# Kernel optimization log

Measured on AMD Instinct MI355X. Metric: run time of the kernel, lower is better.

## Reference

```python
import jax, jax.numpy as jnp
import numpy as np

SEGMENT_LENGTHS = (768, 1536, 3072, 6144, 12288)
DILATED_RATIOS = (1, 2, 4, 8, 16)
NUM_HEADS = 12
NEG_INF = -1e9


def _layer_norm(x, g, b, eps=1e-5):
    mu = jnp.mean(x, axis=-1, keepdims=True)
    var = jnp.mean((x - mu) ** 2, axis=-1, keepdims=True)
    return (x - mu) * jax.lax.rsqrt(var + eps) * g + b


def _dilated_branch(q, k, v, w, r):
    # q,k,v: (B, L, H, Dh); segment length w, dilation ratio r (w % r == 0)
    B, L, H, Dh = q.shape
    Lp = -(-L // w) * w
    n, m = Lp // w, w // r
    gsz = -(-H // r)  # head-group size (heads padded up to a multiple of r in LongNet)
    offs = jnp.arange(H) // gsz  # per-head token offset within each r-block
    oh = jax.nn.one_hot(offs, r, dtype=q.dtype)  # (H, r)

    def gather(t):
        t = jnp.pad(t, ((0, 0), (0, Lp - L), (0, 0), (0, 0)))
        t = t.reshape(B, n, m, r, H, Dh)  # segments of w = m blocks of r
        return jnp.einsum('bnmrhd,hr->bnmhd', t, oh)  # each head picks its offset

    qi, ki, vi = gather(q), gather(k), gather(v)
    s = jnp.einsum('bnihd,bnjhd->bnhij', qi * (Dh ** -0.5), ki)  # (B,n,H,m,m)
    lse = jax.scipy.special.logsumexp(s, axis=-1)  # (B,n,H,m)
    o = jnp.einsum('bnhij,bnjhd->bnihd', jax.nn.softmax(s, axis=-1), vi)
    # scatter back to dense token positions; uncovered slots get 0 / -inf lse
    o_full = jnp.einsum('bnmhd,hr->bnmrhd', o, oh).reshape(B, Lp, H, Dh)
    lse = jnp.transpose(lse, (0, 1, 3, 2))  # (B,n,m,H)
    lse_full = jnp.where(oh.T[None, None, None] > 0, lse[:, :, :, None, :], NEG_INF)
    lse_full = lse_full.reshape(B, Lp, H)
    return o_full[:, :L], lse_full[:, :L]


def _dilated_attention(q, k, v):
    outs, lses = [], []
    for w, r in zip(SEGMENT_LENGTHS, DILATED_RATIOS):
        o, l = _dilated_branch(q, k, v, w, r)
        outs.append(o)
        lses.append(l)
    lse = jnp.stack(lses)  # (n_branch, B, L, H)
    wts = jnp.exp(lse - lse.max(0))
    wts = wts / wts.sum(0)  # softmax-combine branches by their lse (LongNet recombination)
    return (jnp.stack(outs) * wts[..., None]).sum(0)  # (B, L, H, Dh)


def _forward(x, patch_w, patch_b, cls_token, pos_embed,
             ln1_g, ln1_b, wq, bq, wk, bk, wv, bv, wo, bo,
             ln2_g, ln2_b, w1, b1, w2, b2, normf_g, normf_b, head_w, head_b):
    B, Cin, D, Hs, Ws = x.shape
    E = patch_w.shape[0]
    pd, ph, pw = patch_w.shape[2], patch_w.shape[3], patch_w.shape[4]
    # non-overlapping 3D patch embed (Conv3d with stride == kernel)
    xp = x.reshape(B, Cin, D // pd, pd, Hs // ph, ph, Ws // pw, pw)
    tok = jnp.einsum('bcxpyqzr,ecpqr->bxyze', xp, patch_w).reshape(B, -1, E) + patch_b
    tok = tok + pos_embed[:, 1:]
    cls = cls_token + pos_embed[:, :1]
    h = jnp.concatenate([jnp.broadcast_to(cls, (B, 1, E)), tok], axis=1)
    L = h.shape[1]
    Dh = E // NUM_HEADS
    depth = wq.shape[0]
    for i in range(depth):  # pre-LN transformer layers with LongNet dilated attention
        hn = _layer_norm(h, ln1_g[i], ln1_b[i])
        q = (hn @ wq[i] + bq[i]).reshape(B, L, NUM_HEADS, Dh)
        k = (hn @ wk[i] + bk[i]).reshape(B, L, NUM_HEADS, Dh)
        v = (hn @ wv[i] + bv[i]).reshape(B, L, NUM_HEADS, Dh)
        a = _dilated_attention(q, k, v).reshape(B, L, E)
        h = h + a @ wo[i] + bo[i]
        hn = _layer_norm(h, ln2_g[i], ln2_b[i])
        h = h + jax.nn.gelu(hn @ w1[i] + b1[i], approximate=False) @ w2[i] + b2[i]
    h = _layer_norm(h, normf_g, normf_b)
    return h[:, 0] @ head_w + head_b  # (B, num_classes)


def setup_inputs() -> dict:
    key = jax.random.key(0)
    ks = jax.random.split(key, 12)
    B, E, depth, ncls = 2, 768, 2, 1000
    D, Hs, Ws = 48, 256, 256
    N = (D // 4) * (Hs // 16) * (Ws // 16)  # 3072 patches
    f32 = jnp.float32
    s = 0.02
    return {
        'x': jax.random.normal(ks[0], (B, 1, D, Hs, Ws), f32),
        'patch_w': jax.random.normal(ks[1], (E, 1, 4, 16, 16), f32) * s,
        'patch_b': jnp.zeros((E,), f32),
        'cls_token': jax.random.normal(ks[2], (1, 1, E), f32) * s,
        'pos_embed': jax.random.normal(ks[3], (1, N + 1, E), f32) * s,
        'ln1_g': jnp.ones((depth, E), f32),
        'ln1_b': jnp.zeros((depth, E), f32),
        'wq': jax.random.normal(ks[4], (depth, E, E), f32) * s,
        'bq': jnp.zeros((depth, E), f32),
        'wk': jax.random.normal(ks[5], (depth, E, E), f32) * s,
        'bk': jnp.zeros((depth, E), f32),
        'wv': jax.random.normal(ks[6], (depth, E, E), f32) * s,
        'bv': jnp.zeros((depth, E), f32),
        'wo': jax.random.normal(ks[7], (depth, E, E), f32) * s,
        'bo': jnp.zeros((depth, E), f32),
        'ln2_g': jnp.ones((depth, E), f32),
        'ln2_b': jnp.zeros((depth, E), f32),
        'w1': jax.random.normal(ks[8], (depth, E, 4 * E), f32) * s,
        'b1': jnp.zeros((depth, 4 * E), f32),
        'w2': jax.random.normal(ks[9], (depth, 4 * E, E), f32) * s,
        'b2': jnp.zeros((depth, E), f32),
        'normf_g': jnp.ones((E,), f32),
        'normf_b': jnp.zeros((E,), f32),
        'head_w': jax.random.normal(ks[10], (E, ncls), f32) * s,
        'head_b': jnp.zeros((ncls,), f32),
    }


def reference(x, patch_w, patch_b, cls_token, pos_embed,
              ln1_g, ln1_b, wq, bq, wk, bk, wv, bv, wo, bo,
              ln2_g, ln2_b, w1, b1, w2, b2, normf_g, normf_b, head_w, head_b):
    return _forward(x, patch_w, patch_b, cls_token, pos_embed,
                    ln1_g, ln1_b, wq, bq, wk, bk, wv, bv, wo, bo,
                    ln2_g, ln2_b, w1, b1, w2, b2, normf_g, normf_b, head_w, head_b)
```

## Files before the change

kernel.cpp:

```cpp
#include <hip/hip_runtime.h>
#include <math.h>

#define TOK_L 3073
#define EMB 768
#define NH 12
#define DH 64
#define BATCH 2
#define QKVS 2304
#define HSZ ((size_t)BATCH * TOK_L * EMB)
#define MHC ((size_t)BATCH * TOK_L * NH)

typedef __bf16 bf16;
typedef __bf16 v8bf __attribute__((ext_vector_type(8)));
typedef __bf16 v4bf __attribute__((ext_vector_type(4)));
typedef float  v4f  __attribute__((ext_vector_type(4)));

__device__ __forceinline__ v8bf zero8() {
    v8bf v;
    #pragma unroll
    for (int i = 0; i < 8; i++) v[i] = (bf16)0.f;
    return v;
}
__device__ __forceinline__ v4f zero4() {
    v4f v; v[0] = 0.f; v[1] = 0.f; v[2] = 0.f; v[3] = 0.f; return v;
}
__device__ __forceinline__ float gelu_f(float x) {
    return 0.5f * x * (1.0f + erff(x * 0.70710678118654752f));
}
__device__ __forceinline__ void gload16(const bf16* g, bf16* l) {
    __builtin_amdgcn_global_load_lds(
        (const __attribute__((address_space(1))) void*)g,
        (__attribute__((address_space(3))) void*)l, 16, 0, 0);
}

__device__ __forceinline__ void convT_tile(const float* __restrict__ src,
                                           bf16* __restrict__ dst,
                                           int K, int N, int tx, int ty)
{
    __shared__ float t[32][33];
    int n0 = tx * 32, k0 = ty * 32;
    int r = threadIdx.x >> 3, c4 = (threadIdx.x & 7) * 4;
    float4 v = *(const float4*)(src + (size_t)(k0 + r) * N + n0 + c4);
    t[r][c4 + 0] = v.x; t[r][c4 + 1] = v.y; t[r][c4 + 2] = v.z; t[r][c4 + 3] = v.w;
    __syncthreads();
    v4bf o;
    o[0] = (bf16)t[c4 + 0][r]; o[1] = (bf16)t[c4 + 1][r];
    o[2] = (bf16)t[c4 + 2][r]; o[3] = (bf16)t[c4 + 3][r];
    *(v4bf*)(dst + (size_t)(n0 + r) * K + k0 + c4) = o;
}

__global__ __launch_bounds__(256) void prep_weights(
    const float* __restrict__ wq, const float* __restrict__ wk,
    const float* __restrict__ wv, const float* __restrict__ wo,
    const float* __restrict__ w1, const float* __restrict__ w2,
    const float* __restrict__ patch_w,
    bf16* __restrict__ qkv_t0, bf16* __restrict__ wo_t0,
    bf16* __restrict__ w1_t, bf16* __restrict__ w2_t, bf16* __restrict__ pw_b)
{
    int bid = blockIdx.x;
    if (bid >= 13824) {
        int i = ((bid - 13824) * 256 + threadIdx.x) * 4;
        float4 v = *(const float4*)(patch_w + i);
        v4bf o; o[0] = (bf16)v.x; o[1] = (bf16)v.y; o[2] = (bf16)v.z; o[3] = (bf16)v.w;
        *(v4bf*)(pw_b + i) = o;
        return;
    }
    int layer = bid / 6912, t = bid % 6912;
    if (t < 1728) {
        int m = t / 576, tt = t % 576;
        const float* src = (m == 0 ? wq : m == 1 ? wk : wv) + (size_t)layer * 589824;
        bf16* dst = qkv_t0 + (size_t)layer * QKVS * 768 + (size_t)m * 589824;
        convT_tile(src, dst, 768, 768, tt % 24, tt / 24);
    } else if (t < 2304) {
        int tt = t - 1728;
        convT_tile(wo + (size_t)layer * 589824, wo_t0 + (size_t)layer * 589824,
                   768, 768, tt % 24, tt / 24);
    } else if (t < 4608) {
        int tt = t - 2304;
        convT_tile(w1 + (size_t)layer * 2359296, w1_t + (size_t)layer * 2359296,
                   768, 3072, tt % 96, tt / 96);
    } else {
        int tt = t - 4608;
        convT_tile(w2 + (size_t)layer * 2359296, w2_t + (size_t)layer * 2359296,
                   3072, 768, tt % 24, tt / 24);
    }
}

__global__ __launch_bounds__(256) void prep_small(const float* __restrict__ bq,
    const float* __restrict__ bk, const float* __restrict__ bv, float* __restrict__ d,
    const float* __restrict__ cls, const float* __restrict__ pos, float* __restrict__ h)
{
    int i = blockIdx.x * 256 + threadIdx.x;
    if (i < 2 * QKVS) {
        int layer = i / QKVS, j = i % QKVS;
        const float* s = (j < 768) ? bq : (j < 1536) ? bk : bv;
        d[i] = s[(size_t)layer * 768 + (j & 767)];
    }
    if (i < 2 * 768) {
        int b = i / 768, e = i % 768;
        h[(size_t)b * TOK_L * EMB + e] = cls[e] + pos[e];
    }
}

__global__ __launch_bounds__(256) void gather_patches(const float* __restrict__ x,
                                                      bf16* __restrict__ Xp) {
    int p = blockIdx.x;
    int b = p / 3072, pp = p % 3072;
    int px = pp >> 8, py = (pp >> 4) & 15, pz = pp & 15;
    for (int k = threadIdx.x; k < 1024; k += 256) {
        int pd = k >> 8, ph = (k >> 4) & 15, pw = k & 15;
        size_t src = ((size_t)(b * 48 + px * 4 + pd)) * 65536
                   + (size_t)(py * 16 + ph) * 256 + (size_t)(pz * 16 + pw);
        Xp[(size_t)p * 1024 + k] = (bf16)x[src];
    }
}

template<int BN>
__global__ __launch_bounds__(256) void gemm_bf16(
    const bf16* __restrict__ A, const bf16* __restrict__ Bt,
    const float* __restrict__ bias, float* __restrict__ Cf,
    bf16* __restrict__ Cb, int M, int N, int K, int flags,
    const float* __restrict__ pos)
{
    __shared__ bf16 As[128 * 32];
    __shared__ bf16 Bs[BN * 32];
    const int tid = threadIdx.x;
    const int lane = tid & 63, wid = tid >> 6;
    const int ln15 = lane & 15, q4 = lane >> 4;
    const int m0 = blockIdx.y * 128, n0 = blockIdx.x * BN;
    const int wm = (wid & 1) * 64, wn = (wid >> 1) * (BN / 2);
    const int srow = lane >> 2;
    const int schunk = (lane & 3) * 8;
    const int NF = BN / 32;

    v4f acc[4][NF];
    #pragma unroll
    for (int i = 0; i < 4; i++)
        #pragma unroll
        for (int j = 0; j < NF; j++) acc[i][j] = zero4();

    for (int k0 = 0; k0 < K; k0 += 32) {
        #pragma unroll
        for (int i = 0; i < 2; i++) {
            int rg = wid * 32 + i * 16;
            int gm = m0 + rg + srow; if (gm >= M) gm = M - 1;
            gload16(A + (size_t)gm * K + k0 + schunk, As + rg * 32);
        }
        if (BN == 128) {
            #pragma unroll
            for (int i = 0; i < 2; i++) {
                int rg = wid * 32 + i * 16;
                gload16(Bt + (size_t)(n0 + rg + srow) * K + k0 + schunk, Bs + rg * 32);
            }
        } else {
            int rg = wid * 16;
            gload16(Bt + (size_t)(n0 + rg + srow) * K + k0 + schunk, Bs + rg * 32);
        }
        __syncthreads();
        v8bf af[4], bfr[NF];
        #pragma unroll
        for (int mt = 0; mt < 4; mt++)
            af[mt] = *(const v8bf*)(As + (wm + mt * 16 + ln15) * 32 + q4 * 8);
        #pragma unroll
        for (int nt = 0; nt < NF; nt++)
            bfr[nt] = *(const v8bf*)(Bs + (wn + nt * 16 + ln15) * 32 + q4 * 8);
        #pragma unroll
        for (int mt = 0; mt < 4; mt++)
            #pragma unroll
            for (int nt = 0; nt < NF; nt++)
                acc[mt][nt] = __builtin_amdgcn_mfma_f32_16x16x32_bf16(af[mt], bfr[nt], acc[mt][nt], 0, 0, 0);
        __syncthreads();
    }
    #pragma unroll
    for (int mt = 0; mt < 4; mt++) {
        #pragma unroll
        for (int nt = 0; nt < NF; nt++) {
            #pragma unroll
            for (int g = 0; g < 4; g++) {
                int row = m0 + wm + mt * 16 + q4 * 4 + g;
                if (row >= M) continue;
                int col = n0 + wn + nt * 16 + ln15;
                float v = acc[mt][nt][g] + bias[col];
                if (flags & 2) v = gelu_f(v);
                size_t crow;
                if (flags & 4) {
                    int rowp = row % 3072;
                    crow = (size_t)(row + row / 3072 + 1);
                    v += pos[(size_t)(rowp + 1) * EMB + col];
                } else crow = (size_t)row;
                size_t ci = crow * (size_t)N + col;
                if (flags & 8) Cb[ci] = (bf16)v;
                else { if (flags & 1) v += Cf[ci]; Cf[ci] = v; }
            }
        }
    }
}

__global__ __launch_bounds__(256) void layernorm_kernel(
    const float* __restrict__ x, const float* __restrict__ g,
    const float* __restrict__ bb, bf16* __restrict__ y, int nrows)
{
    int row = blockIdx.x;
    if (row >= nrows) return;
    int tid = threadIdx.x;
    const float* xr = x + (size_t)row * EMB;
    float v0 = xr[tid], v1 = xr[tid + 256], v2 = xr[tid + 512];
    __shared__ float red[256];
    red[tid] = v0 + v1 + v2;
    __syncthreads();
    for (int o = 128; o > 0; o >>= 1) { if (tid < o) red[tid] += red[tid + o]; __syncthreads(); }
    float mu = red[0] * (1.f / 768.f);
    __syncthreads();
    float d0 = v0 - mu, d1 = v1 - mu, d2 = v2 - mu;
    red[tid] = d0 * d0 + d1 * d1 + d2 * d2;
    __syncthreads();
    for (int o = 128; o > 0; o >>= 1) { if (tid < o) red[tid] += red[tid + o]; __syncthreads(); }
    float rs = rsqrtf(red[0] * (1.f / 768.f) + 1e-5f);
    bf16* yr = y + (size_t)row * EMB;
    yr[tid]       = (bf16)(d0 * rs * g[tid]       + bb[tid]);
    yr[tid + 256] = (bf16)(d1 * rs * g[tid + 256] + bb[tid + 256]);
    yr[tid + 512] = (bf16)(d2 * rs * g[tid + 512] + bb[tid + 512]);
}

__global__ __launch_bounds__(256) void pack_vt(const bf16* __restrict__ qkv,
                                               bf16* __restrict__ Vt)
{
    __shared__ bf16 t[64 * 65];
    int yy = blockIdx.y;
    int br, seg;
    if (yy < 5)       { br = 0; seg = yy; }
    else if (yy < 8)  { br = 1; seg = yy - 5; }
    else if (yy < 10) { br = 2; seg = yy - 8; }
    else if (yy == 10){ br = 3; seg = 0; }
    else              { br = 4; seg = 0; }
    const int r = 1 << br, w = 768 << br;
    const int gsz = (NH + r - 1) / r;
    const int bh = blockIdx.z;
    const int b = bh / NH, hd = bh % NH;
    const int off = hd / gsz;
    const int kbase = seg * w + off;
    const int kt = blockIdx.x;
    const int tid = threadIdx.x;
    const int dq = (tid & 7) * 8;
    #pragma unroll
    for (int p = 0; p < 2; p++) {
        int jl = (tid >> 3) + p * 32;
        int pk = kbase + (kt * 64 + jl) * r;
        v8bf val = (pk < TOK_L)
            ? *(const v8bf*)(qkv + (size_t)(b * TOK_L + pk) * QKVS + 1536 + hd * DH + dq)
            : zero8();
        #pragma unroll
        for (int i = 0; i < 8; i++) t[jl * 65 + dq + i] = val[i];
    }
    __syncthreads();
    #pragma unroll
    for (int p = 0; p < 2; p++) {
        int d = (tid >> 3) + p * 32;
        int kk = (tid & 7) * 8;
        v8bf o;
        #pragma unroll
        for (int i = 0; i < 8; i++) o[i] = t[(kk + i) * 65 + d];
        *(v8bf*)(Vt + ((size_t)(yy * 24 + bh) * 64 + d) * 768 + kt * 64 + kk) = o;
    }
}

__global__ __launch_bounds__(256) void attn_mfma(
    const bf16* __restrict__ qkv, const bf16* __restrict__ Vt,
    bf16* __restrict__ oac, bf16* __restrict__ obr, float* __restrict__ lse5)
{
    __shared__ bf16 kl[2 * 4096];
    __shared__ bf16 pl[4][32 * 72];
    const int tid = threadIdx.x;
    const int lane = tid & 63, wid = tid >> 6;
    const int ln15 = lane & 15, q4 = lane >> 4;
    const int bid = blockIdx.x;
    const int xcd = bid & 7, rest = bid >> 3;
    const int slot = rest / 6, t = rest - slot * 6;
    const int g = (slot << 3) | xcd;
    const int yy = g / 24, bh = g - yy * 24;
    int br, seg;
    if (yy < 5)       { br = 0; seg = yy; }
    else if (yy < 8)  { br = 1; seg = yy - 5; }
    else if (yy < 10) { br = 2; seg = yy - 8; }
    else if (yy == 10){ br = 3; seg = 0; }
    else              { br = 4; seg = 0; }
    const int r = 1 << br, w = 768 << br;
    const int gsz = (NH + r - 1) / r;
    const int b = bh / NH, hd = bh % NH;
    const int off = hd / gsz;
    const int sbase = seg * w + off;
    if (sbase + (t * 128) * r >= TOK_L) return;

    int n_valid = (TOK_L - sbase + r - 1) / r;
    if (n_valid > 768) n_valid = 768;
    const int kt_lim = (n_valid + 63) >> 6;
    const float pad_add = (float)(768 - n_valid);
    const int qoff = t * 128 + wid * 32;
    const bool wactive = (sbase + qoff * r) < TOK_L;

    const bf16* qb_ = qkv + hd * DH;
    const bf16* kb_ = qkv + 768 + hd * DH;

    auto stageK = [&](int ktv, int bufi) {
        #pragma unroll
        for (int p = 0; p < 2; p++) {
            int row = (tid >> 3) + p * 32;
            int pk = sbase + (ktv * 64 + row) * r;
            if (pk >= TOK_L) pk = 0;
            gload16(kb_ + (size_t)(b * TOK_L + pk) * QKVS + (tid & 7) * 8,
                    kl + bufi * 4096 + wid * 512 + p * 2048);
        }
    };

    v8bf qf[2][2];
    #pragma unroll
    for (int mt = 0; mt < 2; mt++) {
        int pq = sbase + (qoff + mt * 16 + ln15) * r;
        #pragma unroll
        for (int ks = 0; ks < 2; ks++) {
            v8bf qv = (pq < TOK_L)
                ? *(const v8bf*)(qb_ + (size_t)(b * TOK_L + pq) * QKVS + ks * 32 + q4 * 8)
                : zero8();
            #pragma unroll
            for (int i = 0; i < 8; i++) qv[i] = (bf16)((float)qv[i] * 0.125f);
            qf[mt][ks] = qv;
        }
    }
    v4f o[2][4];
    float lsum[2][4];
    #pragma unroll
    for (int mt = 0; mt < 2; mt++)
        #pragma unroll
        for (int g2 = 0; g2 < 4; g2++) { lsum[mt][g2] = 0.f; o[mt][g2] = zero4(); }
    #pragma unroll
    for (int mt = 0; mt < 2; mt++)
        #pragma unroll
        for (int dt = 0; dt < 4; dt++) o[mt][dt] = zero4();

    const bf16* vtb = Vt + (size_t)(yy * 24 + bh) * 64 * 768;
    bf16* plw = &pl[wid][0];

    stageK(0, 0);
    __syncthreads();

    for (int kt = 0; kt < kt_lim; kt++) {
        const int cur = kt & 1;
        if (kt + 1 < kt_lim) stageK(kt + 1, cur ^ 1);
        if (wactive) {
            const bf16* klc = kl + cur * 4096;
            v8bf kf[4][2];
            #pragma unroll
            for (int nt = 0; nt < 4; nt++)
                #pragma unroll
                for (int ks = 0; ks < 2; ks++)
                    kf[nt][ks] = *(const v8bf*)(klc + (nt * 16 + ln15) * 64 + ks * 32 + q4 * 8);
            v4f s[2][4];
            #pragma unroll
            for (int mt = 0; mt < 2; mt++)
                #pragma unroll
                for (int nt = 0; nt < 4; nt++) {
                    s[mt][nt] = __builtin_amdgcn_mfma_f32_16x16x32_bf16(qf[mt][0], kf[nt][0], zero4(), 0, 0, 0);
                    s[mt][nt] = __builtin_amdgcn_mfma_f32_16x16x32_bf16(qf[mt][1], kf[nt][1], s[mt][nt], 0, 0, 0);
                }
            bool vm[4];
            #pragma unroll
            for (int nt = 0; nt < 4; nt++)
                vm[nt] = (kt * 64 + nt * 16 + ln15) < n_valid;
            #pragma unroll
            for (int mt = 0; mt < 2; mt++) {
                #pragma unroll
                for (int g2 = 0; g2 < 4; g2++) {
                    int rowq = mt * 16 + q4 * 4 + g2;
                    #pragma unroll
                    for (int nt = 0; nt < 4; nt++) {
                        float p = vm[nt] ? __expf(s[mt][nt][g2]) : 0.f;
                        lsum[mt][g2] += p;
                        plw[rowq * 72 + nt * 16 + ln15] = (bf16)p;
                    }
                }
            }
            #pragma unroll
            for (int ks = 0; ks < 2; ks++) {
                v8bf pa[2], vf[4];
                #pragma unroll
                for (int mt = 0; mt < 2; mt++)
                    pa[mt] = *(const v8bf*)(plw + (mt * 16 + ln15) * 72 + ks * 32 + q4 * 8);
                #pragma unroll
                for (int dt = 0; dt < 4; dt++)
                    vf[dt] = *(const v8bf*)(vtb + (size_t)(dt * 16 + ln15) * 768 + kt * 64 + ks * 32 + q4 * 8);
                #pragma unroll
                for (int mt = 0; mt < 2; mt++)
                    #pragma unroll
                    for (int dt = 0; dt < 4; dt++)
                        o[mt][dt] = __builtin_amdgcn_mfma_f32_16x16x32_bf16(pa[mt], vf[dt], o[mt][dt], 0, 0, 0);
            }
        }
        __syncthreads();
    }
    if (!wactive) return;

    bf16* od = (br == 0) ? oac : obr + (size_t)(br - 1) * HSZ;
    #pragma unroll
    for (int mt = 0; mt < 2; mt++) {
        #pragma unroll
        for (int g2 = 0; g2 < 4; g2++) {
            float l = lsum[mt][g2];
            l += __shfl_xor(l, 1, 64);
            l += __shfl_xor(l, 2, 64);
            l += __shfl_xor(l, 4, 64);
            l += __shfl_xor(l, 8, 64);
            l += pad_add;
            int row = mt * 16 + q4 * 4 + g2;
            int pq = sbase + (qoff + row) * r;
            if (pq >= TOK_L) continue;
            float linv = 1.f / l;
            if (ln15 == 0)
                lse5[(size_t)br * MHC + (size_t)(b * TOK_L + pq) * NH + hd] = __logf(l);
            #pragma unroll
            for (int dt = 0; dt < 4; dt++)
                od[(size_t)(b * TOK_L + pq) * EMB + hd * DH + dt * 16 + ln15] =
                    (bf16)(o[mt][dt][g2] * linv);
        }
    }
}

__global__ __launch_bounds__(256) void attn_combine(
    const bf16* __restrict__ oac, const bf16* __restrict__ obr,
    const float* __restrict__ lse5, bf16* __restrict__ outb)
{
    size_t e = (size_t)blockIdx.x * 256 + threadIdx.x;
    if (e >= HSZ) return;
    size_t g = e >> 6;
    int h = (int)(g % NH);
    int p = (int)((g / NH) % TOK_L);
    float l0 = lse5[g];
    float m = l0;
    float lv[4];
    bool cov[4];
    #pragma unroll
    for (int j = 0; j < 4; j++) {
        int r = 2 << j;
        int gsz = (NH + r - 1) / r;
        cov[j] = ((p & (r - 1)) == (h / gsz));
        if (cov[j]) {
            lv[j] = lse5[(size_t)(j + 1) * MHC + g];
            m = fmaxf(m, lv[j]);
        }
    }
    float w0 = __expf(l0 - m);
    float wsum = w0;
    float acc = w0 * (float)oac[e];
    #pragma unroll
    for (int j = 0; j < 4; j++) {
        if (cov[j]) {
            float wj = __expf(lv[j] - m);
            wsum += wj;
            acc = fmaf(wj, (float)obr[(size_t)j * HSZ + e], acc);
        }
    }
    outb[e] = (bf16)(acc / wsum);
}

__global__ __launch_bounds__(256) void head_kernel(
    const bf16* __restrict__ hn, const float* __restrict__ hw,
    const float* __restrict__ hb, float* __restrict__ out)
{
    int b = blockIdx.y;
    int c = blockIdx.x * 256 + threadIdx.x;
    __shared__ float srow[EMB];
    for (int e = threadIdx.x; e < EMB; e += 256)
        srow[e] = (float)hn[(size_t)b * TOK_L * EMB + e];
    __syncthreads();
    if (c < 1000) {
        float acc = hb[c];
        for (int e = 0; e < EMB; e++)
            acc = fmaf(srow[e], hw[(size_t)e * 1000 + c], acc);
        out[b * 1000 + c] = acc;
    }
}

extern "C" void kernel_launch(void* const* d_in, const int* in_sizes, int n_in,
                              void* d_out, int out_size, void* d_ws, size_t ws_size,
                              hipStream_t stream)
{
    const float* x       = (const float*)d_in[0];
    const float* patch_w = (const float*)d_in[1];
    const float* patch_b = (const float*)d_in[2];
    const float* cls_tok = (const float*)d_in[3];
    const float* pos_emb = (const float*)d_in[4];
    const float* ln1_g   = (const float*)d_in[5];
    const float* ln1_b   = (const float*)d_in[6];
    const float* wq      = (const float*)d_in[7];
    const float* bq      = (const float*)d_in[8];
    const float* wk      = (const float*)d_in[9];
    const float* bk      = (const float*)d_in[10];
    const float* wv      = (const float*)d_in[11];
    const float* bv      = (const float*)d_in[12];
    const float* wo      = (const float*)d_in[13];
    const float* bo      = (const float*)d_in[14];
    const float* ln2_g   = (const float*)d_in[15];
    const float* ln2_b   = (const float*)d_in[16];
    const float* w1      = (const float*)d_in[17];
    const float* b1      = (const float*)d_in[18];
    const float* w2      = (const float*)d_in[19];
    const float* b2      = (const float*)d_in[20];
    const float* normf_g = (const float*)d_in[21];
    const float* normf_b = (const float*)d_in[22];
    const float* head_w  = (const float*)d_in[23];
    const float* head_b  = (const float*)d_in[24];
    float* out = (float*)d_out;

    char* wp = (char*)d_ws;
    auto alloc = [&](size_t bytes) { char* r = wp; wp += (bytes + 255) & ~(size_t)255; return r; };
    float* h    = (float*)alloc(HSZ * 4);
    bf16*  hn   = (bf16*)alloc(HSZ * 2);
    bf16*  QKV  = (bf16*)alloc((size_t)BATCH * TOK_L * QKVS * 2);
    bf16*  oac  = (bf16*)alloc(HSZ * 2);
    float* lse5 = (float*)alloc(5 * MHC * 4);
    bf16*  Vt   = (bf16*)alloc((size_t)12 * 24 * 64 * 768 * 2);
    bf16*  mid  = (bf16*)alloc(4 * HSZ * 2);
    bf16*  obr  = mid;
    bf16*  Xp   = mid;

    bf16*  qkv_t0 = (bf16*)alloc((size_t)2 * QKVS * 768 * 2);
    bf16*  wo_t0  = (bf16*)alloc((size_t)2 * 768 * 768 * 2);
    bf16*  w1_t   = (bf16*)alloc((size_t)2 * 3072 * 768 * 2);
    bf16*  w2_t   = (bf16*)alloc((size_t)2 * 768 * 3072 * 2);
    bf16*  pw_b   = (bf16*)alloc((size_t)768 * 1024 * 2);
    float* bqkv   = (float*)alloc((size_t)2 * QKVS * 4);

    const int M = BATCH * TOK_L;
    const int MT = (M + 127) / 128;

    prep_weights<<<dim3(14592), 256, 0, stream>>>(wq, wk, wv, wo, w1, w2, patch_w,
                                                  qkv_t0, wo_t0, w1_t, w2_t, pw_b);
    prep_small<<<dim3(18), 256, 0, stream>>>(bq, bk, bv, bqkv, cls_tok, pos_emb, h);

    gather_patches<<<dim3(BATCH * 3072), 256, 0, stream>>>(x, Xp);
    gemm_bf16<64><<<dim3(12, 48), 256, 0, stream>>>(Xp, pw_b, patch_b, h, nullptr,
                                                    BATCH * 3072, 768, 1024, 4, pos_emb);

    for (int layer = 0; layer < 2; layer++) {
        size_t bOff  = (size_t)layer * 768;
        size_t b1Off = (size_t)layer * 3072;
        bf16* qt   = qkv_t0 + (size_t)layer * QKVS * 768;
        bf16* wo_t = wo_t0 + (size_t)layer * 589824;

        layernorm_kernel<<<dim3(M), 256, 0, stream>>>(h, ln1_g + bOff, ln1_b + bOff, hn, M);
        gemm_bf16<128><<<dim3(18, MT), 256, 0, stream>>>(hn, qt, bqkv + (size_t)layer * QKVS,
                                                         nullptr, QKV, M, QKVS, 768, 8, nullptr);

        pack_vt<<<dim3(12, 12, 24), 256, 0, stream>>>(QKV, Vt);
        attn_mfma<<<dim3(1728), 256, 0, stream>>>(QKV, Vt, oac, obr, lse5);
        attn_combine<<<dim3((unsigned)((HSZ + 255) / 256)), 256, 0, stream>>>(oac, obr, lse5, hn);

        gemm_bf16<64><<<dim3(12, MT), 256, 0, stream>>>(hn, wo_t, bo + bOff, h, nullptr,
                                                        M, 768, 768, 1, nullptr);

        layernorm_kernel<<<dim3(M), 256, 0, stream>>>(h, ln2_g + bOff, ln2_b + bOff, hn, M);
        gemm_bf16<128><<<dim3(24, MT), 256, 0, stream>>>(hn, w1_t + (size_t)layer * 2359296, b1 + b1Off,
                                                         nullptr, mid, M, 3072, 768, 8 | 2, nullptr);
        gemm_bf16<64><<<dim3(12, MT), 256, 0, stream>>>(mid, w2_t + (size_t)layer * 2359296, b2 + bOff,
                                                        h, nullptr, M, 768, 3072, 1, nullptr);
    }

    layernorm_kernel<<<dim3(M), 256, 0, stream>>>(h, normf_g, normf_b, hn, M);
    head_kernel<<<dim3(4, BATCH), 256, 0, stream>>>(hn, head_w, head_b, out);
}
```

Before: 1.056 ms.

## Keep attention probabilities in registers via transposed QK MFMA and permlane swaps

Computes S transposed (K as the A operand) so each lane holds four consecutive keys for one query, packs exp values to bf16 with v_cvt_pk_bf16_f32, and rearranges them with permlane32/16 swaps directly into the A-operand layout for the PV MFMA. This removes the per-wave LDS round trip for P and shrinks the row-sum to two shuffles. It also XOR-swizzles the K tile in LDS to reduce bank conflicts on the fragment reads. The result depends on the permlane layout mapping being exactly right.

After: 1.039 ms. Within noise of the previous version (-1.6%).

```diff
diff --git a/kernel.cpp b/kernel.cpp
--- a/kernel.cpp
+++ b/kernel.cpp
@@ -14,6 +14,7 @@
 typedef __bf16 v8bf __attribute__((ext_vector_type(8)));
 typedef __bf16 v4bf __attribute__((ext_vector_type(4)));
 typedef float  v4f  __attribute__((ext_vector_type(4)));
+typedef unsigned int v4u __attribute__((ext_vector_type(4)));
 
 __device__ __forceinline__ v8bf zero8() {
     v8bf v;
@@ -269,7 +270,6 @@
     bf16* __restrict__ oac, bf16* __restrict__ obr, float* __restrict__ lse5)
 {
     __shared__ bf16 kl[2 * 4096];
-    __shared__ bf16 pl[4][32 * 72];
     const int tid = threadIdx.x;
     const int lane = tid & 63, wid = tid >> 6;
     const int ln15 = lane & 15, q4 = lane >> 4;
@@ -301,13 +301,16 @@
     const bf16* qb_ = qkv + hd * DH;
     const bf16* kb_ = qkv + 768 + hd * DH;
 
+    const int swz = (ln15 & 7) * 8;
+
     auto stageK = [&](int ktv, int bufi) {
         #pragma unroll
         for (int p = 0; p < 2; p++) {
             int row = (tid >> 3) + p * 32;
             int pk = sbase + (ktv * 64 + row) * r;
             if (pk >= TOK_L) pk = 0;
-            gload16(kb_ + (size_t)(b * TOK_L + pk) * QKVS + (tid & 7) * 8,
+            int colsw = ((tid & 7) ^ ((tid >> 3) & 7)) * 8;
+            gload16(kb_ + (size_t)(b * TOK_L + pk) * QKVS + colsw,
                     kl + bufi * 4096 + wid * 512 + p * 2048);
         }
     };
@@ -327,18 +330,15 @@
         }
     }
     v4f o[2][4];
-    float lsum[2][4];
-    #pragma unroll
-    for (int mt = 0; mt < 2; mt++)
-        #pragma unroll
-        for (int g2 = 0; g2 < 4; g2++) { lsum[mt][g2] = 0.f; o[mt][g2] = zero4(); }
-    #pragma unroll
-    for (int mt = 0; mt < 2; mt++)
+    float lsum[2];
+    #pragma unroll
+    for (int mt = 0; mt < 2; mt++) {
+        lsum[mt] = 0.f;
         #pragma unroll
         for (int dt = 0; dt < 4; dt++) o[mt][dt] = zero4();
+    }
 
     const bf16* vtb = Vt + (size_t)(yy * 24 + bh) * 64 * 768;
-    bf16* plw = &pl[wid][0];
 
     stageK(0, 0);
     __syncthreads();
@@ -353,69 +353,88 @@
             for (int nt = 0; nt < 4; nt++)
                 #pragma unroll
                 for (int ks = 0; ks < 2; ks++)
-                    kf[nt][ks] = *(const v8bf*)(klc + (nt * 16 + ln15) * 64 + ks * 32 + q4 * 8);
-            v4f s[2][4];
-            #pragma unroll
-            for (int mt = 0; mt < 2; mt++)
+                    kf[nt][ks] = *(const v8bf*)(klc + (nt * 16 + ln15) * 64
+                                                + ((ks * 32 + q4 * 8) ^ swz));
+            unsigned int paw[2][2][4];
+            #pragma unroll
+            for (int mt = 0; mt < 2; mt++) {
+                v4f s[4];
                 #pragma unroll
                 for (int nt = 0; nt < 4; nt++) {
-                    s[mt][nt] = __builtin_amdgcn_mfma_f32_16x16x32_bf16(qf[mt][0], kf[nt][0], zero4(), 0, 0, 0);
-                    s[mt][nt] = __builtin_amdgcn_mfma_f32_16x16x32_bf16(qf[mt][1], kf[nt][1], s[mt][nt], 0, 0, 0);
+                    s[nt] = __builtin_amdgcn_mfma_f32_16x16x32_bf16(kf[nt][0], qf[mt][0], zero4(), 0, 0, 0);
+                    s[nt] = __builtin_amdgcn_mfma_f32_16x16x32_bf16(kf[nt][1], qf[mt][1], s[nt], 0, 0, 0);
                 }
-            bool vm[4];
-            #pragma unroll
-            for (int nt = 0; nt < 4; nt++)
-                vm[nt] = (kt * 64 + nt * 16 + ln15) < n_valid;
-            #pragma unroll
-            for (int mt = 0; mt < 2; mt++) {
+                unsigned int W[4][2];
+                float ls = 0.f;
                 #pragma unroll
-                for (int g2 = 0; g2 < 4; g2++) {
-                    int rowq = mt * 16 + q4 * 4 + g2;
+                for (int nt = 0; nt < 4; nt++) {
+                    int kb = kt * 64 + nt * 16 + q4 * 4;
+                    float p0 = (kb + 0 < n_valid) ? __expf(s[nt][0]) : 0.f;
+                    float p1 = (kb + 1 < n_valid) ? __expf(s[nt][1]) : 0.f;
+                    float p2 = (kb + 2 < n_valid) ? __expf(s[nt][2]) : 0.f;
+                    float p3 = (kb + 3 < n_valid) ? __expf(s[nt][3]) : 0.f;
+                    ls += (p0 + p1) + (p2 + p3);
+                    asm("v_cvt_pk_bf16_f32 %0, %1, %2" : "=v"(W[nt][0]) : "v"(p0), "v"(p1));
+                    asm("v_cvt_pk_bf16_f32 %0, %1, %2" : "=v"(W[nt][1]) : "v"(p2), "v"(p3));
+                }
+                lsum[mt] += ls;
+                #pragma unroll
+                for (int ks = 0; ks < 2; ks++) {
                     #pragma unroll
-                    for (int nt = 0; nt < 4; nt++) {
-                        float p = vm[nt] ? __expf(s[mt][nt][g2]) : 0.f;
-                        lsum[mt][g2] += p;
-                        plw[rowq * 72 + nt * 16 + ln15] = (bf16)p;
+                    for (int h = 0; h < 2; h++) {
+                        unsigned int a = W[2 * ks][h], c = W[2 * ks + 1][h];
+                        asm("v_permlane32_swap_b32 %0, %1" : "+v"(a), "+v"(c));
+                        asm("v_permlane16_swap_b32 %0, %1" : "+v"(a), "+v"(c));
+                        paw[mt][ks][h]     = a;
+                        paw[mt][ks][2 + h] = c;
                     }
                 }
             }
             #pragma unroll
             for (int ks = 0; ks < 2; ks++) {
-                v8bf pa[2], vf[4];
-                #pragma unroll
-                for (int mt = 0; mt < 2; mt++)
-                    pa[mt] = *(const v8bf*)(plw + (mt * 16 + ln15) * 72 + ks * 32 + q4 * 8);
+                v8bf vf[4];
                 #pragma unroll
                 for (int dt = 0; dt < 4; dt++)
                     vf[dt] = *(const v8bf*)(vtb + (size_t)(dt * 16 + ln15) * 768 + kt * 64 + ks * 32 + q4 * 8);
                 #pragma unroll
-                for (int mt = 0; mt < 2; mt++)
+                for (int mt = 0; mt < 2; mt++) {
+                    v4u pw = { paw[mt][ks][0], paw[mt][ks][1], paw[mt][ks][2], paw[mt][ks][3] };
+                    v8bf pa = __builtin_bit_cast(v8bf, pw);
                     #pragma unroll
                     for (int dt = 0; dt < 4; dt++)
-                        o[mt][dt] = __builtin_amdgcn_mfma_f32_16x16x32_bf16(pa[mt], vf[dt], o[mt][dt], 0, 0, 0);
+                        o[mt][dt] = __builtin_amdgcn_mfma_f32_16x16x32_bf16(pa, vf[dt], o[mt][dt], 0, 0, 0);
+                }
             }
         }
         __syncthreads();
     }
     if (!wactive) return;
 
+    float lf[2];
+    #pragma unroll
+    for (int mt = 0; mt < 2; mt++) {
+        float l = lsum[mt];
+        l += __shfl_xor(l, 16, 64);
+        l += __shfl_xor(l, 32, 64);
+        l += pad_add;
+        lf[mt] = l;
+        if (q4 == 0) {
+            int pq = sbase + (qoff + mt * 16 + ln15) * r;
+            if (pq < TOK_L)
+                lse5[(size_t)br * MHC + (size_t)(b * TOK_L + pq) * NH + hd] = __logf(l);
+        }
+    }
+
     bf16* od = (br == 0) ? oac : obr + (size_t)(br - 1) * HSZ;
     #pragma unroll
     for (int mt = 0; mt < 2; mt++) {
         #pragma unroll
         for (int g2 = 0; g2 < 4; g2++) {
-            float l = lsum[mt][g2];
-            l += __shfl_xor(l, 1, 64);
-            l += __shfl_xor(l, 2, 64);
-            l += __shfl_xor(l, 4, 64);
-            l += __shfl_xor(l, 8, 64);
-            l += pad_add;
+            float l = __shfl(lf[mt], q4 * 4 + g2, 64);
             int row = mt * 16 + q4 * 4 + g2;
             int pq = sbase + (qoff + row) * r;
             if (pq >= TOK_L) continue;
             float linv = 1.f / l;
-            if (ln15 == 0)
-                lse5[(size_t)br * MHC + (size_t)(b * TOK_L + pq) * NH + hd] = __logf(l);
             #pragma unroll
             for (int dt = 0; dt < 4; dt++)
                 od[(size_t)(b * TOK_L + pq) * EMB + hd * DH + dt * 16 + ln15] =
```
